# Kernel optimization log

Measured on AMD Instinct MI355X. Metric: run time of the kernel, lower is better.

## Reference

```python
import jax, jax.numpy as jnp
import numpy as np

K = 4096  # num_embeddings
D = 256   # embedding_dim

def setup_inputs() -> dict:
    key = jax.random.key(0)
    k1, k2 = jax.random.split(key)
    z_e = jax.random.normal(k1, (32, 32, 32, 256), dtype=jnp.float32)
    embedding = jax.random.normal(k2, (K, D), dtype=jnp.float32)
    return {"z_e": z_e, "embedding": embedding}

def reference(z_e, embedding):
    # z_e: [B,H,W,D] channels-last; embedding: [K,D]
    B, H, W, Dd = z_e.shape
    z_flat = z_e.reshape(-1, Dd)                                   # [N,D]
    # squared L2 distances via expansion: ||z||^2 + ||e||^2 - 2 z.e
    distances = (jnp.sum(z_flat**2, axis=1, keepdims=True)
                 + jnp.sum(embedding**2, axis=1)
                 - 2.0 * jnp.matmul(z_flat, embedding.T))          # [N,K]
    indices = jnp.argmin(distances, axis=1)                        # [N]
    z_q = embedding[indices].reshape(B, H, W, Dd)                  # gather
    # straight-through estimator
    z_q = z_e + jax.lax.stop_gradient(z_q - z_e)
    # perplexity (codebook utilization)
    avg_probs = jnp.bincount(indices, length=K).astype(jnp.float32) / indices.shape[0]
    perplexity = jnp.exp(-jnp.sum(avg_probs * jnp.log(avg_probs + 1e-10)))
    return z_q, indices.reshape(B, H, W), perplexity
```

## Files before the change

kernel.cpp:

```cpp
#include <hip/hip_runtime.h>
#include <hip/hip_bf16.h>
#include <math.h>
#include <stdint.h>

typedef _Float16 f16;
typedef _Float16 f16x8 __attribute__((ext_vector_type(8)));
typedef float f32x16 __attribute__((ext_vector_type(16)));

#define DIM 256
#define LOSCALE 2048.0f
#define INV_LOSCALE (1.0f/2048.0f)

#define BP_BYTES (4096u*1024u + 16384u)

#define GLOAD16(gp, lp) __builtin_amdgcn_global_load_lds( \
    (const __attribute__((address_space(1))) void*)(gp),  \
    (__attribute__((address_space(3))) void*)(lp), 16, 0, 0)

__global__ void vq_pack2(const float* __restrict__ emb, f16* __restrict__ bp)
{
    int o = blockIdx.x * blockDim.x + threadIdx.x;
    int l = o & 63;
    int b = o >> 6;
    int t   = b & 1;
    int s   = (b >> 1) & 15;
    int col = b >> 5;
    int code  = col * 32 + (l & 31);
    int depth = s * 16 + (l >> 5) * 8;
    const float* gp = emb + (size_t)code * DIM + depth;
    float4 x0 = *(const float4*)gp;
    float4 x1 = *(const float4*)(gp + 4);
    float xs[8] = {x0.x, x0.y, x0.z, x0.w, x1.x, x1.y, x1.z, x1.w};
    f16x8 v;
    #pragma unroll
    for (int j = 0; j < 8; ++j) {
        f16 h = (f16)xs[j];
        v[j] = t ? (f16)((xs[j] - (float)h) * LOSCALE) : h;
    }
    *(f16x8*)(bp + (size_t)o * 8) = v;
}

__global__ void vq_e2(const float* __restrict__ emb, float* __restrict__ e2) {
    int k = blockIdx.x;
    int l = threadIdx.x;
    float4 v = ((const float4*)(emb + (size_t)k * DIM))[l];
    float s = v.x * v.x + v.y * v.y + v.z * v.z + v.w * v.w;
    #pragma unroll
    for (int off = 32; off; off >>= 1) s += __shfl_xor(s, off);
    if (l == 0) e2[k] = s;
}

__global__ void vq_zero(int* __restrict__ p, int n) {
    int i = blockIdx.x * blockDim.x + threadIdx.x;
    if (i < n) p[i] = 0;
}

__global__ __launch_bounds__(256, 2) void vq_argmin6(
    const float* __restrict__ z, const char* __restrict__ bp,
    const float* __restrict__ e2, unsigned long long* __restrict__ part)
{
    __shared__ __align__(16) char lds[2][32768];

    const int t    = threadIdx.x;
    const int lane = t & 63;
    const int rt   = t >> 6;
    const int hw   = blockIdx.x & 1;
    const int rg   = blockIdx.x >> 1;
    const int l31  = lane & 31;
    const int hi5  = lane >> 5;
    const int rowbase = rg * 128 + rt * 32;

    f16x8 a_h[16], a_l[16];
    {
        const float* zr = z + (size_t)(rowbase + l31) * DIM + hi5 * 8;
        #pragma unroll
        for (int s = 0; s < 16; ++s) {
            float4 x0 = *(const float4*)(zr + s * 16);
            float4 x1 = *(const float4*)(zr + s * 16 + 4);
            float xs[8] = {x0.x, x0.y, x0.z, x0.w, x1.x, x1.y, x1.z, x1.w};
            #pragma unroll
            for (int j = 0; j < 8; ++j) {
                f16 h = (f16)xs[j];
                a_h[s][j] = h;
                a_l[s][j] = (f16)((xs[j] - (float)h) * LOSCALE);
            }
        }
    }

    float    bestd[16];
    unsigned bcol[4];
    #pragma unroll
    for (int q = 0; q < 16; ++q) bestd[q] = 3.4e38f;
    #pragma unroll
    for (int i = 0; i < 4; ++i) bcol[i] = 0u;

    const char* bhalf = bp + ((size_t)hw << 21);

#define STAGE(pb, cc) do {                                                    \
    const char* src_ = bhalf + ((size_t)(cc) << 15) + (size_t)t * 16;         \
    char* dst_ = lds[pb] + t * 16;                                            \
    _Pragma("unroll")                                                         \
    for (int i_ = 0; i_ < 8; ++i_)                                            \
        GLOAD16(src_ + i_ * 4096, dst_ + i_ * 4096);                          \
    } while (0)

    STAGE(0, 0);
    __syncthreads();
    int cur = 0;

    for (int c = 0; c < 64; ++c) {
        if (c < 63) STAGE(cur ^ 1, c + 1);

        float e2c = e2[hw * 2048 + c * 32 + l31];
        f32x16 acc0, acc1a, acc1b;
        #pragma unroll
        for (int q = 0; q < 16; ++q) { acc0[q] = 0.0f; acc1a[q] = 0.0f; acc1b[q] = 0.0f; }

        const char* bb = lds[cur];
        __builtin_amdgcn_s_setprio(1);
        #pragma unroll
        for (int s = 0; s < 16; ++s) {
            f16x8 bh = *(const f16x8*)(bb + s * 2048 + lane * 16);
            f16x8 bl = *(const f16x8*)(bb + s * 2048 + 1024 + lane * 16);
            acc0  = __builtin_amdgcn_mfma_f32_32x32x16_f16(a_h[s], bh, acc0,  0, 0, 0);
            acc1a = __builtin_amdgcn_mfma_f32_32x32x16_f16(a_h[s], bl, acc1a, 0, 0, 0);
            acc1b = __builtin_amdgcn_mfma_f32_32x32x16_f16(a_l[s], bh, acc1b, 0, 0, 0);
        }
        __builtin_amdgcn_s_setprio(0);

        #pragma unroll
        for (int q = 0; q < 16; ++q) {
            float dot  = fmaf(acc1a[q] + acc1b[q], INV_LOSCALE, acc0[q]);
            float dist = fmaf(-2.0f, dot, e2c);
            bool  lt   = dist < bestd[q];
            bestd[q]   = lt ? dist : bestd[q];
            const unsigned sh = (unsigned)((q & 3) * 8);
            unsigned nv = (bcol[q >> 2] & ~(0xFFu << sh)) | ((unsigned)c << sh);
            bcol[q >> 2] = lt ? nv : bcol[q >> 2];
        }

        __syncthreads();
        cur ^= 1;
    }
#undef STAGE

    #pragma unroll
    for (int q = 0; q < 16; ++q) {
        float    d = bestd[q];
        unsigned c = (unsigned)(hw * 2048) +
                     ((bcol[q >> 2] >> ((q & 3) * 8)) & 0xFFu) * 32u + (unsigned)l31;
        #pragma unroll
        for (int o2 = 16; o2; o2 >>= 1) {
            float    od = __shfl_xor(d, o2);
            unsigned oc = __shfl_xor(c, o2);
            if (od < d || (od == d && oc < c)) { d = od; c = oc; }
        }
        if (l31 == 0) {
            int row = (q & 3) + 8 * (q >> 2) + 4 * hi5;
            unsigned u   = __float_as_uint(d);
            unsigned key = u ^ (unsigned)(((int)u >> 31) | 0x80000000);
            part[(size_t)hw * 32768 + rowbase + row] =
                ((unsigned long long)key << 32) | c;
        }
    }
}

__global__ void vq_combine(const unsigned long long* __restrict__ part,
                           float* __restrict__ idxf, int N)
{
    int i = blockIdx.x * blockDim.x + threadIdx.x;
    if (i >= N) return;
    unsigned long long a = part[i];
    unsigned long long b = part[(size_t)N + i];
    unsigned long long m = b < a ? b : a;
    idxf[i] = (float)(unsigned)(m & 0xffffffffu);
}

__global__ __launch_bounds__(256, 2) void vq_argmin_f32(
    const float* __restrict__ z, const float* __restrict__ emb,
    const float* __restrict__ e2, float* __restrict__ idxf, int K)
{
    __shared__ float zs[64 * 36];
    __shared__ float es[128 * 36];
    const int t = threadIdx.x;
    const int tx = t & 15;
    const int ty = t >> 4;
    const int rowbase = blockIdx.x * 64;
    const float* zbase = z + (size_t)rowbase * DIM;
    float best[4]; int bidx[4];
    #pragma unroll
    for (int i = 0; i < 4; ++i) { best[i] = 3.4e38f; bidx[i] = 0; }
    for (int kt = 0; kt < K; kt += 128) {
        float acc[4][8];
        #pragma unroll
        for (int i = 0; i < 4; ++i)
            #pragma unroll
            for (int j = 0; j < 8; ++j) acc[i][j] = 0.0f;
        for (int dc = 0; dc < DIM; dc += 32) {
            { int lr = t >> 2, o = (t & 3) * 8;
              const float* gp = zbase + (size_t)lr * DIM + dc + o;
              *(float4*)&zs[lr*36+o]   = *(const float4*)gp;
              *(float4*)&zs[lr*36+o+4] = *(const float4*)(gp+4); }
            { int lc = t >> 1, o = (t & 1) * 16;
              const float* gp = emb + (size_t)(kt+lc) * DIM + dc + o;
              *(float4*)&es[lc*36+o]    = *(const float4*)gp;
              *(float4*)&es[lc*36+o+4]  = *(const float4*)(gp+4);
              *(float4*)&es[lc*36+o+8]  = *(const float4*)(gp+8);
              *(float4*)&es[lc*36+o+12] = *(const float4*)(gp+12); }
            __syncthreads();
            const float* zp = &zs[(ty*4)*36];
            const float* ep = &es[tx*36];
            #pragma unroll
            for (int d = 0; d < 32; d += 4) {
                float4 zv[4], ev[8];
                #pragma unroll
                for (int i = 0; i < 4; ++i) zv[i] = *(const float4*)&zp[i*36+d];
                #pragma unroll
                for (int j = 0; j < 8; ++j) ev[j] = *(const float4*)&ep[j*16*36+d];
                #pragma unroll
                for (int i = 0; i < 4; ++i)
                    #pragma unroll
                    for (int j = 0; j < 8; ++j) {
                        acc[i][j] += zv[i].x*ev[j].x; acc[i][j] += zv[i].y*ev[j].y;
                        acc[i][j] += zv[i].z*ev[j].z; acc[i][j] += zv[i].w*ev[j].w;
                    }
            }
            __syncthreads();
        }
        #pragma unroll
        for (int j = 0; j < 8; ++j) {
            int c = kt + tx + 16*j;
            float ev2 = e2[c];
            #pragma unroll
            for (int i = 0; i < 4; ++i) {
                float dist = ev2 - 2.0f*acc[i][j];
                if (dist < best[i] || (dist == best[i] && c < bidx[i])) { best[i]=dist; bidx[i]=c; }
            }
        }
    }
    #pragma unroll
    for (int i = 0; i < 4; ++i) {
        float bd = best[i]; int bi = bidx[i];
        #pragma unroll
        for (int off = 8; off; off >>= 1) {
            float od = __shfl_xor(bd, off); int oi = __shfl_xor(bi, off);
            if (od < bd || (od == bd && oi < bi)) { bd = od; bi = oi; }
        }
        if (tx == 0) idxf[rowbase + ty*4 + i] = (float)bi;
    }
}

__global__ void vq_gather(const float* __restrict__ emb,
                          const float* __restrict__ idxf,
                          float* __restrict__ zq, int N)
{
    int n = blockIdx.x * 4 + (threadIdx.x >> 6);
    int l = threadIdx.x & 63;
    if (n >= N) return;
    int idx = (int)idxf[n];
    ((float4*)(zq + (size_t)n * DIM))[l] = ((const float4*)(emb + (size_t)idx * DIM))[l];
}

__global__ void vq_hist(const float* __restrict__ idxf, int* __restrict__ counts, int N) {
    int n = blockIdx.x * blockDim.x + threadIdx.x;
    if (n < N) atomicAdd(&counts[(int)idxf[n]], 1);
}

__global__ void vq_ppl(const int* __restrict__ counts, float invN,
                       float* __restrict__ out, int K)
{
    int t = threadIdx.x;
    float s = 0.0f;
    for (int k = t; k < K; k += 256) {
        float p = (float)counts[k] * invN;
        s += p * logf(p + 1e-10f);
    }
    #pragma unroll
    for (int off = 32; off; off >>= 1) s += __shfl_xor(s, off);
    __shared__ float wsum[4];
    if ((t & 63) == 0) wsum[t >> 6] = s;
    __syncthreads();
    if (t == 0) out[0] = expf(-(wsum[0] + wsum[1] + wsum[2] + wsum[3]));
}

extern "C" void kernel_launch(void* const* d_in, const int* in_sizes, int n_in,
                              void* d_out, int out_size, void* d_ws, size_t ws_size,
                              hipStream_t stream)
{
    const float* z   = (const float*)d_in[0];
    const float* emb = (const float*)d_in[1];
    const int N = in_sizes[0] / DIM;
    const int K = in_sizes[1] / DIM;

    float* out  = (float*)d_out;
    float* zq   = out;
    float* idxf = out + (size_t)N * DIM;
    float* ppl  = idxf + N;

    const size_t PART_BYTES = 2ull * 32768 * sizeof(unsigned long long);
    const size_t NEED = (size_t)BP_BYTES + 16384 + 16384 + PART_BYTES;

    if (ws_size >= NEED && K == 4096 && N == 32768) {
        f16*   bpk    = (f16*)d_ws;
        float* e2     = (float*)((char*)d_ws + BP_BYTES);
        int*   counts = (int*)((char*)d_ws + BP_BYTES + 16384);
        unsigned long long* part =
            (unsigned long long*)((char*)d_ws + BP_BYTES + 32768);

        vq_pack2<<<1024, 256, 0, stream>>>(emb, bpk);
        vq_e2<<<K, 64, 0, stream>>>(emb, e2);
        vq_zero<<<(K + 255) / 256, 256, 0, stream>>>(counts, K);
        vq_argmin6<<<(N / 128) * 2, 256, 0, stream>>>(z, (const char*)bpk, e2, part);
        vq_combine<<<N / 256, 256, 0, stream>>>(part, idxf, N);
        vq_gather<<<N / 4, 256, 0, stream>>>(emb, idxf, zq, N);
        vq_hist<<<(N + 255) / 256, 256, 0, stream>>>(idxf, counts, N);
        vq_ppl<<<1, 256, 0, stream>>>(counts, 1.0f / (float)N, ppl, K);
    } else {
        float* e2     = (float*)d_ws;
        int*   counts = (int*)((char*)d_ws + (size_t)K * sizeof(float));
        vq_e2<<<K, 64, 0, stream>>>(emb, e2);
        vq_zero<<<(K + 255) / 256, 256, 0, stream>>>(counts, K);
        vq_argmin_f32<<<N / 64, 256, 0, stream>>>(z, emb, e2, idxf, K);
        vq_gather<<<N / 4, 256, 0, stream>>>(emb, idxf, zq, N);
        vq_hist<<<(N + 255) / 256, 256, 0, stream>>>(idxf, counts, N);
        vq_ppl<<<1, 256, 0, stream>>>(counts, 1.0f / (float)N, ppl, K);
    }
}
```

Baseline: 242.7 us.

## Deepen codebook LDS pipeline to four half-size buffers with split barriers

Splits each 32 KB codebook chunk into two 16 KB units staged into a four-deep ring of LDS buffers. Loads now run two units ahead, and explicit vmcnt waits with raw s_barrier replace the full __syncthreads per chunk, so global-to-LDS copies overlap MFMA work more deeply. It also preloads this block's half of e2 into LDS and software-prefetches B fragments from LDS into registers inside the MFMA loop. The costs are extra LDS (about 72 KB per block), the risk of tighter occupancy, and a padded workspace to cover the over-staged tail units.

```diff
diff --git a/kernel.cpp b/kernel.cpp
--- a/kernel.cpp
+++ b/kernel.cpp
@@ -11,7 +11,7 @@
 #define LOSCALE 2048.0f
 #define INV_LOSCALE (1.0f/2048.0f)
 
-#define BP_BYTES (4096u*1024u + 16384u)
+#define BP_BYTES (4096u*1024u + 32768u)
 
 #define GLOAD16(gp, lp) __builtin_amdgcn_global_load_lds( \
     (const __attribute__((address_space(1))) void*)(gp),  \
@@ -55,11 +55,12 @@
     if (i < n) p[i] = 0;
 }
 
-__global__ __launch_bounds__(256, 2) void vq_argmin6(
+__global__ __launch_bounds__(256, 2) void vq_argmin7(
     const float* __restrict__ z, const char* __restrict__ bp,
     const float* __restrict__ e2, unsigned long long* __restrict__ part)
 {
-    __shared__ __align__(16) char lds[2][32768];
+    __shared__ __align__(16) char bufs[4][16384];
+    __shared__ float e2s[2048];
 
     const int t    = threadIdx.x;
     const int lane = t & 63;
@@ -69,6 +70,9 @@
     const int l31  = lane & 31;
     const int hi5  = lane >> 5;
     const int rowbase = rg * 128 + rt * 32;
+
+    *(float4*)&e2s[t * 8]     = *(const float4*)(e2 + hw * 2048 + t * 8);
+    *(float4*)&e2s[t * 8 + 4] = *(const float4*)(e2 + hw * 2048 + t * 8 + 4);
 
     f16x8 a_h[16], a_l[16];
     {
@@ -86,6 +90,7 @@
             }
         }
     }
+    __syncthreads();
 
     float    bestd[16];
     unsigned bcol[4];
@@ -96,37 +101,57 @@
 
     const char* bhalf = bp + ((size_t)hw << 21);
 
-#define STAGE(pb, cc) do {                                                    \
-    const char* src_ = bhalf + ((size_t)(cc) << 15) + (size_t)t * 16;         \
-    char* dst_ = lds[pb] + t * 16;                                            \
+#define STAGE(pb, uu) do {                                                    \
+    const char* src_ = bhalf + ((size_t)(uu) << 14) + (size_t)t * 16;         \
+    char* dst_ = bufs[pb] + t * 16;                                           \
     _Pragma("unroll")                                                         \
-    for (int i_ = 0; i_ < 8; ++i_)                                            \
+    for (int i_ = 0; i_ < 4; ++i_)                                            \
         GLOAD16(src_ + i_ * 4096, dst_ + i_ * 4096);                          \
     } while (0)
 
+#define COMPUTE8(BB, SB) do {                                                 \
+    const char* bbp_ = (BB);                                                  \
+    f16x8 bh_ = *(const f16x8*)(bbp_ + lane * 16);                            \
+    f16x8 bl_ = *(const f16x8*)(bbp_ + 1024 + lane * 16);                     \
+    __builtin_amdgcn_s_setprio(1);                                            \
+    _Pragma("unroll")                                                         \
+    for (int sl_ = 0; sl_ < 8; ++sl_) {                                       \
+        f16x8 bhn_, bln_;                                                     \
+        if (sl_ < 7) {                                                        \
+            bhn_ = *(const f16x8*)(bbp_ + (sl_+1) * 2048 + lane * 16);        \
+            bln_ = *(const f16x8*)(bbp_ + (sl_+1) * 2048 + 1024 + lane * 16); \
+        }                                                                     \
+        acc0  = __builtin_amdgcn_mfma_f32_32x32x16_f16(a_h[(SB)+sl_], bh_, acc0,  0,0,0); \
+        acc1a = __builtin_amdgcn_mfma_f32_32x32x16_f16(a_h[(SB)+sl_], bl_, acc1a, 0,0,0); \
+        acc1b = __builtin_amdgcn_mfma_f32_32x32x16_f16(a_l[(SB)+sl_], bh_, acc1b, 0,0,0); \
+        if (sl_ < 7) { bh_ = bhn_; bl_ = bln_; }                              \
+    }                                                                         \
+    __builtin_amdgcn_s_setprio(0);                                            \
+    } while (0)
+
+#define PHASE_SYNC() do {                                                     \
+    asm volatile("s_waitcnt vmcnt(8)" ::: "memory");                          \
+    asm volatile("s_waitcnt lgkmcnt(0)" ::: "memory");                        \
+    __builtin_amdgcn_s_barrier();                                             \
+    __builtin_amdgcn_sched_barrier(0);                                        \
+    } while (0)
+
     STAGE(0, 0);
-    __syncthreads();
-    int cur = 0;
+    STAGE(1, 1);
 
     for (int c = 0; c < 64; ++c) {
-        if (c < 63) STAGE(cur ^ 1, c + 1);
-
-        float e2c = e2[hw * 2048 + c * 32 + l31];
+        float e2c = e2s[c * 32 + l31];
         f32x16 acc0, acc1a, acc1b;
         #pragma unroll
         for (int q = 0; q < 16; ++q) { acc0[q] = 0.0f; acc1a[q] = 0.0f; acc1b[q] = 0.0f; }
 
-        const char* bb = lds[cur];
-        __builtin_amdgcn_s_setprio(1);
-        #pragma unroll
-        for (int s = 0; s < 16; ++s) {
-            f16x8 bh = *(const f16x8*)(bb + s * 2048 + lane * 16);
-            f16x8 bl = *(const f16x8*)(bb + s * 2048 + 1024 + lane * 16);
-            acc0  = __builtin_amdgcn_mfma_f32_32x32x16_f16(a_h[s], bh, acc0,  0, 0, 0);
-            acc1a = __builtin_amdgcn_mfma_f32_32x32x16_f16(a_h[s], bl, acc1a, 0, 0, 0);
-            acc1b = __builtin_amdgcn_mfma_f32_32x32x16_f16(a_l[s], bh, acc1b, 0, 0, 0);
-        }
-        __builtin_amdgcn_s_setprio(0);
+        STAGE((2*c + 2) & 3, 2*c + 2);
+        PHASE_SYNC();
+        COMPUTE8(bufs[(2*c) & 3], 0);
+
+        STAGE((2*c + 3) & 3, 2*c + 3);
+        PHASE_SYNC();
+        COMPUTE8(bufs[(2*c + 1) & 3], 8);
 
         #pragma unroll
         for (int q = 0; q < 16; ++q) {
@@ -138,11 +163,10 @@
             unsigned nv = (bcol[q >> 2] & ~(0xFFu << sh)) | ((unsigned)c << sh);
             bcol[q >> 2] = lt ? nv : bcol[q >> 2];
         }
-
-        __syncthreads();
-        cur ^= 1;
     }
 #undef STAGE
+#undef COMPUTE8
+#undef PHASE_SYNC
 
     #pragma unroll
     for (int q = 0; q < 16; ++q) {
@@ -310,7 +334,7 @@
         vq_pack2<<<1024, 256, 0, stream>>>(emb, bpk);
         vq_e2<<<K, 64, 0, stream>>>(emb, e2);
         vq_zero<<<(K + 255) / 256, 256, 0, stream>>>(counts, K);
-        vq_argmin6<<<(N / 128) * 2, 256, 0, stream>>>(z, (const char*)bpk, e2, part);
+        vq_argmin7<<<(N / 128) * 2, 256, 0, stream>>>(z, (const char*)bpk, e2, part);
         vq_combine<<<N / 256, 256, 0, stream>>>(part, idxf, N);
         vq_gather<<<N / 4, 256, 0, stream>>>(emb, idxf, zq, N);
         vq_hist<<<(N + 255) / 256, 256, 0, stream>>>(idxf, counts, N);
```

Result: no change. 241.0 us (-0.7%).

## Deepen argmin LDS pipeline to four stages and fuse combine, gather and histogram

Applied to the files above, without the earlier changes.

The argmin kernel now uses 512-thread blocks covering 256 rows each. It keeps a four-buffer LDS ring with prefetch distance two, gated by explicit vmcnt waits and raw barriers instead of a full __syncthreads per step. It also caches the codebook norms in LDS and software-pipelines the LDS fragment reads ahead of the MFMAs. Separately, the combine, gather and histogram kernels are merged into one pass, which removes two launches and the round trip of the index buffer. The exchange is a larger LDS footprint (about 136KB per block, likely one block per CU) and speculative prefetches past the end of the packed codebook, covered by enlarging the workspace padding.

```diff
diff --git a/kernel.cpp b/kernel.cpp
--- a/kernel.cpp
+++ b/kernel.cpp
@@ -11,7 +11,7 @@
 #define LOSCALE 2048.0f
 #define INV_LOSCALE (1.0f/2048.0f)
 
-#define BP_BYTES (4096u*1024u + 16384u)
+#define BP_BYTES (4096u*1024u + 98304u)
 
 #define GLOAD16(gp, lp) __builtin_amdgcn_global_load_lds( \
     (const __attribute__((address_space(1))) void*)(gp),  \
@@ -55,20 +55,23 @@
     if (i < n) p[i] = 0;
 }
 
-__global__ __launch_bounds__(256, 2) void vq_argmin6(
+__global__ __launch_bounds__(512, 2) void vq_argmin9(
     const float* __restrict__ z, const char* __restrict__ bp,
     const float* __restrict__ e2, unsigned long long* __restrict__ part)
 {
-    __shared__ __align__(16) char lds[2][32768];
+    __shared__ __align__(16) char bufs[4][32768];
+    __shared__ float e2s[2048];
 
     const int t    = threadIdx.x;
     const int lane = t & 63;
-    const int rt   = t >> 6;
+    const int wv   = t >> 6;
     const int hw   = blockIdx.x & 1;
     const int rg   = blockIdx.x >> 1;
     const int l31  = lane & 31;
     const int hi5  = lane >> 5;
-    const int rowbase = rg * 128 + rt * 32;
+    const int rowbase = rg * 256 + wv * 32;
+
+    *(float4*)&e2s[t * 4] = *(const float4*)(e2 + hw * 2048 + t * 4);
 
     f16x8 a_h[16], a_l[16];
     {
@@ -87,6 +90,20 @@
         }
     }
 
+    const char* bhalf = bp + ((size_t)hw << 21);
+
+#define STAGE(pb, cc) do {                                                    \
+    const char* src_ = bhalf + ((size_t)(cc) << 15) + (size_t)t * 16;         \
+    char* dst_ = bufs[pb] + t * 16;                                           \
+    _Pragma("unroll")                                                         \
+    for (int i_ = 0; i_ < 4; ++i_)                                            \
+        GLOAD16(src_ + i_ * 8192, dst_ + i_ * 8192);                          \
+    } while (0)
+
+    STAGE(0, 0);
+    STAGE(1, 1);
+    __syncthreads();
+
     float    bestd[16];
     unsigned bcol[4];
     #pragma unroll
@@ -94,40 +111,37 @@
     #pragma unroll
     for (int i = 0; i < 4; ++i) bcol[i] = 0u;
 
-    const char* bhalf = bp + ((size_t)hw << 21);
-
-#define STAGE(pb, cc) do {                                                    \
-    const char* src_ = bhalf + ((size_t)(cc) << 15) + (size_t)t * 16;         \
-    char* dst_ = lds[pb] + t * 16;                                            \
-    _Pragma("unroll")                                                         \
-    for (int i_ = 0; i_ < 8; ++i_)                                            \
-        GLOAD16(src_ + i_ * 4096, dst_ + i_ * 4096);                          \
-    } while (0)
-
-    STAGE(0, 0);
-    __syncthreads();
-    int cur = 0;
-
     for (int c = 0; c < 64; ++c) {
-        if (c < 63) STAGE(cur ^ 1, c + 1);
-
-        float e2c = e2[hw * 2048 + c * 32 + l31];
+        STAGE((c + 2) & 3, c + 2);
+
+        asm volatile("s_waitcnt vmcnt(8)" ::: "memory");
+        asm volatile("s_waitcnt lgkmcnt(0)" ::: "memory");
+        __builtin_amdgcn_s_barrier();
+        __builtin_amdgcn_sched_barrier(0);
+
         f32x16 acc0, acc1a, acc1b;
         #pragma unroll
         for (int q = 0; q < 16; ++q) { acc0[q] = 0.0f; acc1a[q] = 0.0f; acc1b[q] = 0.0f; }
 
-        const char* bb = lds[cur];
+        const char* bb = bufs[c & 3];
+        f16x8 bh_ = *(const f16x8*)(bb + lane * 16);
+        f16x8 bl_ = *(const f16x8*)(bb + 1024 + lane * 16);
         __builtin_amdgcn_s_setprio(1);
         #pragma unroll
-        for (int s = 0; s < 16; ++s) {
-            f16x8 bh = *(const f16x8*)(bb + s * 2048 + lane * 16);
-            f16x8 bl = *(const f16x8*)(bb + s * 2048 + 1024 + lane * 16);
-            acc0  = __builtin_amdgcn_mfma_f32_32x32x16_f16(a_h[s], bh, acc0,  0, 0, 0);
-            acc1a = __builtin_amdgcn_mfma_f32_32x32x16_f16(a_h[s], bl, acc1a, 0, 0, 0);
-            acc1b = __builtin_amdgcn_mfma_f32_32x32x16_f16(a_l[s], bh, acc1b, 0, 0, 0);
+        for (int ks = 0; ks < 16; ++ks) {
+            f16x8 bhn_, bln_;
+            if (ks < 15) {
+                bhn_ = *(const f16x8*)(bb + (ks + 1) * 2048 + lane * 16);
+                bln_ = *(const f16x8*)(bb + (ks + 1) * 2048 + 1024 + lane * 16);
+            }
+            acc0  = __builtin_amdgcn_mfma_f32_32x32x16_f16(a_h[ks], bh_, acc0,  0, 0, 0);
+            acc1a = __builtin_amdgcn_mfma_f32_32x32x16_f16(a_h[ks], bl_, acc1a, 0, 0, 0);
+            acc1b = __builtin_amdgcn_mfma_f32_32x32x16_f16(a_l[ks], bh_, acc1b, 0, 0, 0);
+            if (ks < 15) { bh_ = bhn_; bl_ = bln_; }
         }
         __builtin_amdgcn_s_setprio(0);
 
+        float e2c = e2s[c * 32 + l31];
         #pragma unroll
         for (int q = 0; q < 16; ++q) {
             float dot  = fmaf(acc1a[q] + acc1b[q], INV_LOSCALE, acc0[q]);
@@ -138,9 +152,6 @@
             unsigned nv = (bcol[q >> 2] & ~(0xFFu << sh)) | ((unsigned)c << sh);
             bcol[q >> 2] = lt ? nv : bcol[q >> 2];
         }
-
-        __syncthreads();
-        cur ^= 1;
     }
 #undef STAGE
 
@@ -165,15 +176,24 @@
     }
 }
 
-__global__ void vq_combine(const unsigned long long* __restrict__ part,
-                           float* __restrict__ idxf, int N)
-{
-    int i = blockIdx.x * blockDim.x + threadIdx.x;
-    if (i >= N) return;
-    unsigned long long a = part[i];
-    unsigned long long b = part[(size_t)N + i];
+__global__ void vq_final(const unsigned long long* __restrict__ part,
+                         const float* __restrict__ emb,
+                         float* __restrict__ idxf, float* __restrict__ zq,
+                         int* __restrict__ counts, int N)
+{
+    int n = blockIdx.x * 4 + (threadIdx.x >> 6);
+    int l = threadIdx.x & 63;
+    if (n >= N) return;
+    unsigned long long a = part[n];
+    unsigned long long b = part[(size_t)N + n];
     unsigned long long m = b < a ? b : a;
-    idxf[i] = (float)(unsigned)(m & 0xffffffffu);
+    int idx = (int)(unsigned)(m & 0xffffffffu);
+    ((float4*)(zq + (size_t)n * DIM))[l] =
+        ((const float4*)(emb + (size_t)idx * DIM))[l];
+    if (l == 0) {
+        idxf[n] = (float)idx;
+        atomicAdd(&counts[idx], 1);
+    }
 }
 
 __global__ __launch_bounds__(256, 2) void vq_argmin_f32(
@@ -310,10 +330,8 @@
         vq_pack2<<<1024, 256, 0, stream>>>(emb, bpk);
         vq_e2<<<K, 64, 0, stream>>>(emb, e2);
         vq_zero<<<(K + 255) / 256, 256, 0, stream>>>(counts, K);
-        vq_argmin6<<<(N / 128) * 2, 256, 0, stream>>>(z, (const char*)bpk, e2, part);
-        vq_combine<<<N / 256, 256, 0, stream>>>(part, idxf, N);
-        vq_gather<<<N / 4, 256, 0, stream>>>(emb, idxf, zq, N);
-        vq_hist<<<(N + 255) / 256, 256, 0, stream>>>(idxf, counts, N);
+        vq_argmin9<<<(N / 256) * 2, 512, 0, stream>>>(z, (const char*)bpk, e2, part);
+        vq_final<<<N / 4, 256, 0, stream>>>(part, emb, idxf, zq, counts, N);
         vq_ppl<<<1, 256, 0, stream>>>(counts, 1.0f / (float)N, ppl, K);
     } else {
         float* e2     = (float*)d_ws;
```

Result: faster. 223.5 us (-7.9%).
